# Kernel tuning notes

Hardware: AMD Instinct MI355X
Metric: run time of the kernel (lower is better)

Reference implementation:

```python
import jax, jax.numpy as jnp
import numpy as np

WINDOW = 4
EPS = 1e-5


def setup_inputs() -> dict:
    key = jax.random.key(0)
    ks = jax.random.split(key, 12)
    B, T, D = 2, 4096, 1024
    H = D // 2
    s = 0.02
    return {
        "x": jax.random.normal(ks[0], (B, T, D), dtype=jnp.float32),
        # tension_net: Linear(2D -> D/2), SiLU, Linear(D/2 -> 1). Weights stored [in, out].
        "w1": jax.random.normal(ks[1], (2 * D, H), dtype=jnp.float32) * s,
        "b1": jnp.zeros((H,), dtype=jnp.float32),
        "w2": jax.random.normal(ks[2], (H, 1), dtype=jnp.float32) * s,
        "b2": jnp.zeros((1,), dtype=jnp.float32),
        # wv: Linear(D -> D)
        "wv_w": jax.random.normal(ks[3], (D, D), dtype=jnp.float32) * s,
        "wv_b": jnp.zeros((D,), dtype=jnp.float32),
        # merge: Linear(2D -> D)
        "merge_w": jax.random.normal(ks[4], (2 * D, D), dtype=jnp.float32) * s,
        "merge_b": jnp.zeros((D,), dtype=jnp.float32),
        # LayerNorm(D)
        "gamma": jnp.ones((D,), dtype=jnp.float32),
        "beta": jnp.zeros((D,), dtype=jnp.float32),
    }


def reference(x, w1, b1, w2, b2, wv_w, wv_b, merge_w, merge_b, gamma, beta):
    B, T, D = x.shape
    W = WINDOW
    # Causal sliding-window neighbor gather: nb[:, t, w] = x[:, t-w-1] if t-w-1 >= 0 else 0.
    idx = jnp.arange(T)[:, None] - jnp.arange(W)[None, :] - 1          # [T, W]
    valid = (idx >= 0)                                                  # [T, W]
    nb = jnp.take(x, jnp.clip(idx, 0, None), axis=1)                   # [B, T, W, D]
    nb = jnp.where(valid[None, :, :, None], nb, jnp.zeros((), x.dtype))
    # Pairwise tension gate: tiny MLP on [h_t, nb].
    h_t = jnp.broadcast_to(x[:, :, None, :], (B, T, W, D))
    pair = jnp.concatenate([h_t, nb], axis=-1)                          # [B, T, W, 2D]
    hid = jax.nn.silu(jnp.einsum('btwe,eh->btwh', pair, w1) + b1)       # [B, T, W, D/2]
    tau = jax.nn.sigmoid((jnp.einsum('btwh,ho->btwo', hid, w2) + b2)[..., 0])  # [B, T, W]
    # Value projection of neighbors (note: zero-padded neighbors still get wv bias, matching torch).
    v = jnp.einsum('btwd,de->btwe', nb, wv_w) + wv_b                    # [B, T, W, D]
    msg = jnp.einsum('btw,btwd->btd', tau, v)                           # [B, T, D]
    # Merge + LayerNorm.
    y = jnp.einsum('bte,ed->btd', jnp.concatenate([x, msg], axis=-1), merge_w) + merge_b
    mu = jnp.mean(y, axis=-1, keepdims=True)
    var = jnp.mean(jnp.square(y - mu), axis=-1, keepdims=True)
    y = (y - mu) * jax.lax.rsqrt(var + EPS) * gamma + beta
    return y
```

## Files before the change

### kernel.cpp

```cpp
#include <hip/hip_runtime.h>
#include <hip/hip_bf16.h>

#define TT 4096
#define TD 1024
#define TM 8192
#define CN 3072
#define EPS 1e-5f

typedef __bf16 bf16;
typedef __bf16 bf16x4 __attribute__((ext_vector_type(4)));
typedef __bf16 bf16x8 __attribute__((ext_vector_type(8)));
typedef float  f32x4  __attribute__((ext_vector_type(4)));

#define GLOBAL_AS __attribute__((address_space(1)))
#define LDS_AS    __attribute__((address_space(3)))

__global__ __launch_bounds__(256) void prep_kernel(const float* __restrict__ x,
                                                   const float* __restrict__ w1,
                                                   const float* __restrict__ wv_w,
                                                   const float* __restrict__ wv_b,
                                                   const float* __restrict__ merge_w,
                                                   bf16* __restrict__ Xbf,
                                                   bf16* __restrict__ BigBT,
                                                   bf16* __restrict__ Amb,
                                                   bf16* __restrict__ WvBf,
                                                   float* __restrict__ cvecP) {
    __shared__ float tile[32][33];
    int b = blockIdx.x;
    const int tid = threadIdx.x;

    if (b < 16) {
        const int j = (b & 3) * 256 + tid;
        const int e0 = (b >> 2) * 256;
        const float* col = merge_w + (size_t)(1024 + e0) * 1024 + j;
        float acc = 0.f;
#pragma unroll 32
        for (int e = 0; e < 256; ++e) acc += wv_b[e0 + e] * col[(size_t)e * 1024];
        cvecP[(b >> 2) * 1024 + j] = acc;
        return;
    }
    b -= 16;
    if (b < 8192) {
        int i = b * 256 + tid;
        float4 v = ((const float4*)x)[i];
        bf16x4 o; o[0] = (bf16)v.x; o[1] = (bf16)v.y; o[2] = (bf16)v.z; o[3] = (bf16)v.w;
        *(bf16x4*)(Xbf + (size_t)i * 4) = o;
        return;
    }
    b -= 8192;

    const float* src; bf16* dst; int srcN, tilesX, dstOff;
    if (b < 512)       {            src = w1;                        srcN = 512;  tilesX = 16; dst = BigBT; dstOff = 0;    }
    else if (b < 1024) { b -= 512;  src = w1 + (size_t)1024 * 512;   srcN = 512;  tilesX = 16; dst = BigBT; dstOff = 512;  }
    else if (b < 2048) { b -= 1024; src = merge_w;                   srcN = 1024; tilesX = 32; dst = BigBT; dstOff = 2048; }
    else if (b < 3072) { b -= 2048; src = merge_w + (size_t)1024 * 1024; srcN = 1024; tilesX = 32; dst = Amb; dstOff = 0; }
    else {
        b -= 3072;
        int i = b * 256 + tid;
        float4 v = ((const float4*)wv_w)[i];
        bf16x4 o; o[0] = (bf16)v.x; o[1] = (bf16)v.y; o[2] = (bf16)v.z; o[3] = (bf16)v.w;
        *(bf16x4*)(WvBf + (size_t)i * 4) = o;
        return;
    }
    int n0 = (b % tilesX) * 32, k0 = (b / tilesX) * 32;
    int tx = tid & 31, ty = tid >> 5;
#pragma unroll
    for (int r = 0; r < 32; r += 8)
        tile[ty + r][tx] = src[(size_t)(k0 + ty + r) * srcN + n0 + tx];
    __syncthreads();
#pragma unroll
    for (int r = 0; r < 32; r += 8)
        dst[(size_t)(dstOff + n0 + ty + r) * 1024 + k0 + tx] = (bf16)tile[tx][ty + r];
}

__global__ __launch_bounds__(256) void wprime_kernel(const bf16* __restrict__ Amb,
                                                     const bf16* __restrict__ WvBf,
                                                     bf16* __restrict__ Wout,
                                                     const float* __restrict__ cvecP,
                                                     float* __restrict__ cvec) {
    int b = blockIdx.x;
    if (b == 256) {
        int j = threadIdx.x * 4;
        float4 s0 = *(const float4*)(cvecP + j);
        float4 s1 = *(const float4*)(cvecP + 1024 + j);
        float4 s2 = *(const float4*)(cvecP + 2048 + j);
        float4 s3 = *(const float4*)(cvecP + 3072 + j);
        float4 o = {s0.x + s1.x + s2.x + s3.x, s0.y + s1.y + s2.y + s3.y,
                    s0.z + s1.z + s2.z + s3.z, s0.w + s1.w + s2.w + s3.w};
        *(float4*)(cvec + j) = o;
        return;
    }
    __shared__ bf16 As[64 * 64];
    __shared__ bf16 Bs[64 * 64];
    const int m0 = (b >> 4) * 64;
    const int n0 = (b & 15) * 64;
    const int tid = threadIdx.x;
    const int wave = tid >> 6, lane = tid & 63;
    const int wr = (wave >> 1) * 32, wc = (wave & 1) * 32;
    const int lrow = lane & 15, cbase = lane >> 4;
    const int sw = lrow & 7;

    f32x4 acc[2][2] = {};

    for (int k0 = 0; k0 < 1024; k0 += 64) {
        __syncthreads();
#pragma unroll
        for (int c = 0; c < 2; ++c) {
            int e = (c * 256 + tid) * 8;
            int row = e >> 6;
            int q = (e >> 3) & 7;
            int gcol = ((q ^ (row & 7)) << 3);
            const bf16* ga = Amb  + (size_t)(m0 + row) * 1024 + k0 + gcol;
            const bf16* gb = WvBf + (size_t)(n0 + row) * 1024 + k0 + gcol;
            __builtin_amdgcn_global_load_lds((const GLOBAL_AS void*)ga,
                                             (LDS_AS void*)(As + e), 16, 0, 0);
            __builtin_amdgcn_global_load_lds((const GLOBAL_AS void*)gb,
                                             (LDS_AS void*)(Bs + e), 16, 0, 0);
        }
        __syncthreads();

#pragma unroll
        for (int kk = 0; kk < 2; ++kk) {
            const int qo = ((cbase + kk * 4) ^ sw) << 3;
            bf16x8 af[2], bfr[2];
#pragma unroll
            for (int i = 0; i < 2; ++i) {
                af[i]  = *(const bf16x8*)(As + (wr + i * 16 + lrow) * 64 + qo);
                bfr[i] = *(const bf16x8*)(Bs + (wc + i * 16 + lrow) * 64 + qo);
            }
#pragma unroll
            for (int i = 0; i < 2; ++i)
#pragma unroll
                for (int j = 0; j < 2; ++j)
                    acc[i][j] = __builtin_amdgcn_mfma_f32_16x16x32_bf16(af[i], bfr[j], acc[i][j], 0, 0, 0);
        }
    }

    const int lr = (lane >> 4) * 4, lc = lane & 15;
#pragma unroll
    for (int i = 0; i < 2; ++i)
#pragma unroll
        for (int j = 0; j < 2; ++j)
#pragma unroll
            for (int r = 0; r < 4; ++r)
                Wout[(size_t)(m0 + wr + i * 16 + lr + r) * 1024 + (n0 + wc + j * 16 + lc)]
                    = (bf16)acc[i][j][r];
}

template <bool SWIZ>
__global__ __launch_bounds__(256) void gemm_bt(const bf16* __restrict__ A, int lda,
                                               const bf16* __restrict__ BT,
                                               bf16* __restrict__ C, int N, int K) {
    __shared__ bf16 As[128 * 64];
    __shared__ bf16 Bs[128 * 64];
    int bx = blockIdx.x, by = blockIdx.y;
    if (SWIZ) {
        int L = by * gridDim.x + bx;
        int xcd = L & 7, idx = L >> 3;
        int nyx = gridDim.y >> 3;
        by = xcd * nyx + idx / gridDim.x;
        bx = idx % gridDim.x;
    }
    const int m0 = by * 128;
    const int n0 = bx * 128;
    const int tid = threadIdx.x;
    const int wave = tid >> 6, lane = tid & 63;
    const int wr = (wave >> 1) * 64, wc = (wave & 1) * 64;
    const int lrow = lane & 15, cbase = lane >> 4;
    const int sw = lrow & 7;

    f32x4 acc[4][4] = {};

    for (int k0 = 0; k0 < K; k0 += 64) {
        __syncthreads();
#pragma unroll
        for (int c = 0; c < 4; ++c) {
            int e = (c * 256 + tid) * 8;
            int row = e >> 6;
            int q = (e >> 3) & 7;
            int gcol = ((q ^ (row & 7)) << 3);
            const bf16* ga = A  + (size_t)(m0 + row) * lda + k0 + gcol;
            const bf16* gb = BT + (size_t)(n0 + row) * K   + k0 + gcol;
            __builtin_amdgcn_global_load_lds((const GLOBAL_AS void*)ga,
                                             (LDS_AS void*)(As + e), 16, 0, 0);
            __builtin_amdgcn_global_load_lds((const GLOBAL_AS void*)gb,
                                             (LDS_AS void*)(Bs + e), 16, 0, 0);
        }
        __syncthreads();

#pragma unroll
        for (int kk = 0; kk < 2; ++kk) {
            const int qo = ((cbase + kk * 4) ^ sw) << 3;
            bf16x8 af[4], bfr[4];
#pragma unroll
            for (int i = 0; i < 4; ++i) {
                af[i]  = *(const bf16x8*)(As + (wr + i * 16 + lrow) * 64 + qo);
                bfr[i] = *(const bf16x8*)(Bs + (wc + i * 16 + lrow) * 64 + qo);
            }
#pragma unroll
            for (int i = 0; i < 4; ++i)
#pragma unroll
                for (int j = 0; j < 4; ++j)
                    acc[i][j] = __builtin_amdgcn_mfma_f32_16x16x32_bf16(af[i], bfr[j], acc[i][j], 0, 0, 0);
        }
    }

    const int lr = (lane >> 4) * 4, lc = lane & 15;
#pragma unroll
    for (int i = 0; i < 4; ++i)
#pragma unroll
        for (int j = 0; j < 4; ++j)
#pragma unroll
            for (int r = 0; r < 4; ++r)
                C[(size_t)(m0 + wr + i * 16 + lr + r) * N + (n0 + wc + j * 16 + lc)]
                    = (bf16)acc[i][j][r];
}

__global__ __launch_bounds__(256) void final_kernel(const bf16* __restrict__ C,
                                                    const float* __restrict__ b1,
                                                    const float* __restrict__ b2,
                                                    const float* __restrict__ w2,
                                                    const float* __restrict__ cvec,
                                                    const float* __restrict__ merge_b,
                                                    const float* __restrict__ gamma,
                                                    const float* __restrict__ beta,
                                                    float* __restrict__ out) {
    const int wave = threadIdx.x >> 6, lane = threadIdx.x & 63;
    const int row = blockIdx.x * 4 + wave;
    const int t = row & (TT - 1);
    const bf16* Crow = C + (size_t)row * CN;

    const int h0 = lane * 8;
    bf16x8 u8 = *(const bf16x8*)(Crow + h0);
    float4 b1a = *(const float4*)(b1 + h0), b1b = *(const float4*)(b1 + h0 + 4);
    float4 w2a = *(const float4*)(w2 + h0), w2b = *(const float4*)(w2 + h0 + 4);
    float u[8] = {(float)u8[0] + b1a.x, (float)u8[1] + b1a.y,
                  (float)u8[2] + b1a.z, (float)u8[3] + b1a.w,
                  (float)u8[4] + b1b.x, (float)u8[5] + b1b.y,
                  (float)u8[6] + b1b.z, (float)u8[7] + b1b.w};
    const float w2v[8] = {w2a.x, w2a.y, w2a.z, w2a.w, w2b.x, w2b.y, w2b.z, w2b.w};

    float partial[4];
#pragma unroll
    for (int w = 0; w < 4; ++w) {
        float p = 0.f;
        if (t >= w + 1) {
            bf16x8 v8 = *(const bf16x8*)(C + (size_t)(row - w - 1) * CN + 512 + h0);
#pragma unroll
            for (int k = 0; k < 8; ++k) {
                float z = u[k] + (float)v8[k];
                p += (z / (1.f + __expf(-z))) * w2v[k];
            }
        } else {
#pragma unroll
            for (int k = 0; k < 8; ++k) {
                float z = u[k];
                p += (z / (1.f + __expf(-z))) * w2v[k];
            }
        }
        partial[w] = p;
    }
#pragma unroll
    for (int w = 0; w < 4; ++w)
#pragma unroll
        for (int off = 1; off < 64; off <<= 1)
            partial[w] += __shfl_xor(partial[w], off, 64);

    const float bias2 = b2[0];
    float taus[4];
#pragma unroll
    for (int w = 0; w < 4; ++w)
        taus[w] = 1.f / (1.f + __expf(-(partial[w] + bias2)));
    const float tsum = taus[0] + taus[1] + taus[2] + taus[3];

    const int d0 = lane * 16;
    bf16x8 y1a = *(const bf16x8*)(Crow + 2048 + d0);
    bf16x8 y1b = *(const bf16x8*)(Crow + 2048 + d0 + 8);
    float v[16];
#pragma unroll
    for (int k = 0; k < 8; ++k) { v[k] = (float)y1a[k]; v[8 + k] = (float)y1b[k]; }
#pragma unroll
    for (int q = 0; q < 4; ++q) {
        float4 cv = *(const float4*)(cvec + d0 + q * 4);
        float4 mb = *(const float4*)(merge_b + d0 + q * 4);
        v[q*4+0] += tsum * cv.x + mb.x; v[q*4+1] += tsum * cv.y + mb.y;
        v[q*4+2] += tsum * cv.z + mb.z; v[q*4+3] += tsum * cv.w + mb.w;
    }
#pragma unroll
    for (int w = 0; w < 4; ++w) {
        if (t >= w + 1) {
            const bf16* Pn = C + (size_t)(row - w - 1) * CN + 1024 + d0;
            bf16x8 pa = *(const bf16x8*)Pn;
            bf16x8 pb = *(const bf16x8*)(Pn + 8);
#pragma unroll
            for (int k = 0; k < 8; ++k) {
                v[k] += taus[w] * (float)pa[k];
                v[8 + k] += taus[w] * (float)pb[k];
            }
        }
    }

    float s = 0.f, ss = 0.f;
#pragma unroll
    for (int k = 0; k < 16; ++k) { s += v[k]; ss += v[k] * v[k]; }
#pragma unroll
    for (int off = 1; off < 64; off <<= 1) {
        s  += __shfl_xor(s, off, 64);
        ss += __shfl_xor(ss, off, 64);
    }
    const float mu = s * (1.f / TD);
    const float var = ss * (1.f / TD) - mu * mu;
    const float r = rsqrtf(var + EPS);

#pragma unroll
    for (int q = 0; q < 4; ++q) {
        float4 g  = *(const float4*)(gamma + d0 + q * 4);
        float4 bt = *(const float4*)(beta + d0 + q * 4);
        float4 o;
        o.x = (v[q*4+0] - mu) * r * g.x + bt.x;
        o.y = (v[q*4+1] - mu) * r * g.y + bt.y;
        o.z = (v[q*4+2] - mu) * r * g.z + bt.z;
        o.w = (v[q*4+3] - mu) * r * g.w + bt.w;
        *(float4*)(out + (size_t)row * TD + d0 + q * 4) = o;
    }
}

extern "C" void kernel_launch(void* const* d_in, const int* in_sizes, int n_in,
                              void* d_out, int out_size, void* d_ws, size_t ws_size,
                              hipStream_t stream) {
    const float* x       = (const float*)d_in[0];
    const float* w1      = (const float*)d_in[1];
    const float* b1      = (const float*)d_in[2];
    const float* w2      = (const float*)d_in[3];
    const float* b2      = (const float*)d_in[4];
    const float* wv_w    = (const float*)d_in[5];
    const float* wv_b    = (const float*)d_in[6];
    const float* merge_w = (const float*)d_in[7];
    const float* merge_b = (const float*)d_in[8];
    const float* gamma   = (const float*)d_in[9];
    const float* beta    = (const float*)d_in[10];
    float* out = (float*)d_out;

    char* ws = (char*)d_ws;
    bf16*  Xbf   = (bf16*)ws;  ws += (size_t)TM * 1024 * 2;
    bf16*  BigBT = (bf16*)ws;  ws += (size_t)CN * 1024 * 2;
    bf16*  Amb   = (bf16*)ws;  ws += (size_t)1024 * 1024 * 2;
    bf16*  WvBf  = (bf16*)ws;  ws += (size_t)1024 * 1024 * 2;
    float* cvecP = (float*)ws; ws += (size_t)4 * 1024 * 4;
    float* cvec  = (float*)ws; ws += (size_t)1024 * 4;
    bf16*  Cbuf  = (bf16*)ws;

    prep_kernel<<<12304, 256, 0, stream>>>(x, w1, wv_w, wv_b, merge_w,
                                           Xbf, BigBT, Amb, WvBf, cvecP);

    wprime_kernel<<<257, 256, 0, stream>>>(Amb, WvBf, BigBT + (size_t)1024 * 1024,
                                           cvecP, cvec);

    gemm_bt<true><<<dim3(CN / 128, TM / 128), 256, 0, stream>>>(
        Xbf, 1024, BigBT, Cbuf, CN, 1024);

    final_kernel<<<TM / 4, 256, 0, stream>>>(Cbuf, b1, b2, w2, cvec, merge_b,
                                             gamma, beta, out);
}
```

Baseline: 202.2 us.

## Retile main GEMM to 256x96 blocks with LDS-staged vectorized epilogue

```diff
diff --git a/kernel.cpp b/kernel.cpp
--- a/kernel.cpp
+++ b/kernel.cpp
@@ -147,73 +147,100 @@
                     = (bf16)acc[i][j][r];
 }
 
-template <bool SWIZ>
-__global__ __launch_bounds__(256) void gemm_bt(const bf16* __restrict__ A, int lda,
-                                               const bf16* __restrict__ BT,
-                                               bf16* __restrict__ C, int N, int K) {
-    __shared__ bf16 As[128 * 64];
-    __shared__ bf16 Bs[128 * 64];
+__global__ __launch_bounds__(256, 2) void gemm_big(const bf16* __restrict__ A,
+                                                   const bf16* __restrict__ BT,
+                                                   bf16* __restrict__ C) {
+    __shared__ bf16 SMEM[28672];
+    bf16* As = SMEM;
+    bf16* Bs = SMEM + 16384;
+    const int NB = 3072, K = 1024;
+
     int bx = blockIdx.x, by = blockIdx.y;
-    if (SWIZ) {
-        int L = by * gridDim.x + bx;
+    {
+        int L = by * 32 + bx;
         int xcd = L & 7, idx = L >> 3;
-        int nyx = gridDim.y >> 3;
-        by = xcd * nyx + idx / gridDim.x;
-        bx = idx % gridDim.x;
-    }
-    const int m0 = by * 128;
-    const int n0 = bx * 128;
+        by = xcd * 4 + (idx >> 5);
+        bx = idx & 31;
+    }
+    const int m0 = by * 256;
+    const int n0 = bx * 96;
     const int tid = threadIdx.x;
     const int wave = tid >> 6, lane = tid & 63;
-    const int wr = (wave >> 1) * 64, wc = (wave & 1) * 64;
+    const int wr = wave * 64;
     const int lrow = lane & 15, cbase = lane >> 4;
     const int sw = lrow & 7;
 
-    f32x4 acc[4][4] = {};
+    f32x4 acc[4][6] = {};
 
     for (int k0 = 0; k0 < K; k0 += 64) {
         __syncthreads();
 #pragma unroll
-        for (int c = 0; c < 4; ++c) {
-            int e = (c * 256 + tid) * 8;
-            int row = e >> 6;
-            int q = (e >> 3) & 7;
-            int gcol = ((q ^ (row & 7)) << 3);
-            const bf16* ga = A  + (size_t)(m0 + row) * lda + k0 + gcol;
-            const bf16* gb = BT + (size_t)(n0 + row) * K   + k0 + gcol;
-            __builtin_amdgcn_global_load_lds((const GLOBAL_AS void*)ga,
-                                             (LDS_AS void*)(As + e), 16, 0, 0);
-            __builtin_amdgcn_global_load_lds((const GLOBAL_AS void*)gb,
-                                             (LDS_AS void*)(Bs + e), 16, 0, 0);
+        for (int c = 0; c < 11; ++c) {
+            if (c < 8) {
+                int e = (c * 256 + tid) * 8;
+                int row = e >> 6;
+                int q = (e >> 3) & 7;
+                int gcol = ((q ^ (row & 7)) << 3);
+                const bf16* ga = A + (size_t)(m0 + row) * K + k0 + gcol;
+                __builtin_amdgcn_global_load_lds((const GLOBAL_AS void*)ga,
+                                                 (LDS_AS void*)(As + e), 16, 0, 0);
+            } else {
+                int e = ((c - 8) * 256 + tid) * 8;
+                int row = e >> 6;
+                int q = (e >> 3) & 7;
+                int gcol = ((q ^ (row & 7)) << 3);
+                const bf16* gb = BT + (size_t)(n0 + row) * K + k0 + gcol;
+                __builtin_amdgcn_global_load_lds((const GLOBAL_AS void*)gb,
+                                                 (LDS_AS void*)(Bs + e), 16, 0, 0);
+            }
         }
         __syncthreads();
 
 #pragma unroll
         for (int kk = 0; kk < 2; ++kk) {
             const int qo = ((cbase + kk * 4) ^ sw) << 3;
-            bf16x8 af[4], bfr[4];
-#pragma unroll
-            for (int i = 0; i < 4; ++i) {
-                af[i]  = *(const bf16x8*)(As + (wr + i * 16 + lrow) * 64 + qo);
-                bfr[i] = *(const bf16x8*)(Bs + (wc + i * 16 + lrow) * 64 + qo);
-            }
+            bf16x8 af[4], bfr[6];
 #pragma unroll
             for (int i = 0; i < 4; ++i)
-#pragma unroll
-                for (int j = 0; j < 4; ++j)
+                af[i] = *(const bf16x8*)(As + (wr + i * 16 + lrow) * 64 + qo);
+#pragma unroll
+            for (int j = 0; j < 6; ++j)
+                bfr[j] = *(const bf16x8*)(Bs + (j * 16 + lrow) * 64 + qo);
+#pragma unroll
+            for (int i = 0; i < 4; ++i)
+#pragma unroll
+                for (int j = 0; j < 6; ++j)
                     acc[i][j] = __builtin_amdgcn_mfma_f32_16x16x32_bf16(af[i], bfr[j], acc[i][j], 0, 0, 0);
         }
     }
 
+    __syncthreads();
+    bf16* ep = SMEM + wave * 6656;
     const int lr = (lane >> 4) * 4, lc = lane & 15;
 #pragma unroll
     for (int i = 0; i < 4; ++i)
 #pragma unroll
-        for (int j = 0; j < 4; ++j)
+        for (int j = 0; j < 6; ++j)
 #pragma unroll
             for (int r = 0; r < 4; ++r)
-                C[(size_t)(m0 + wr + i * 16 + lr + r) * N + (n0 + wc + j * 16 + lc)]
-                    = (bf16)acc[i][j][r];
+                ep[(i * 16 + lr + r) * 104 + (j * 16 + lc)] = (bf16)acc[i][j][r];
+    __syncthreads();
+
+    bf16* Cw = C + (size_t)(m0 + wr) * NB + n0;
+#pragma unroll
+    for (int p = 0; p < 8; ++p) {
+        int R = p * 8 + (lane >> 3);
+        int Ccol = (lane & 7) * 8;
+        bf16x8 v = *(const bf16x8*)(ep + R * 104 + Ccol);
+        *(bf16x8*)(Cw + (size_t)R * NB + Ccol) = v;
+    }
+#pragma unroll
+    for (int p = 0; p < 4; ++p) {
+        int R = p * 16 + (lane >> 2);
+        int Ccol = 64 + (lane & 3) * 8;
+        bf16x8 v = *(const bf16x8*)(ep + R * 104 + Ccol);
+        *(bf16x8*)(Cw + (size_t)R * NB + Ccol) = v;
+    }
 }
 
 __global__ __launch_bounds__(256) void final_kernel(const bf16* __restrict__ C,
@@ -356,8 +383,7 @@
     wprime_kernel<<<257, 256, 0, stream>>>(Amb, WvBf, BigBT + (size_t)1024 * 1024,
                                            cvecP, cvec);
 
-    gemm_bt<true><<<dim3(CN / 128, TM / 128), 256, 0, stream>>>(
-        Xbf, 1024, BigBT, Cbuf, CN, 1024);
+    gemm_big<<<dim3(32, 32), 256, 0, stream>>>(Xbf, BigBT, Cbuf);
 
     final_kernel<<<TM / 4, 256, 0, stream>>>(Cbuf, b1, b2, w2, cvec, merge_b,
                                              gamma, beta, out);
```

New measurement: 195.1 us. -3.5%, faster.
